# Kernel tuning notes

Hardware: AMD Instinct MI355X
Metric: run time of the kernel (lower is better)

## Reference

```python
import jax, jax.numpy as jnp
import numpy as np

B, L, DIM, K, V = 512, 200, 256, 2048, 100000


def setup_inputs() -> dict:
    key = jax.random.key(0)
    k1, k2, k3, k4, k5 = jax.random.split(key, 5)
    return {
        "history_item_ids": jax.random.randint(k1, (B, L), 0, V, dtype=jnp.int32),
        "history_item_masks": jax.random.randint(k2, (B, L), 0, 3, dtype=jnp.int32),
        "embedding_table": jax.random.normal(k3, (V, DIM), dtype=jnp.float32) * 0.1,
        "code_book": jax.random.normal(k4, (K, DIM), dtype=jnp.float32) * 0.1,
        "W_enc": jax.random.normal(k5, (2 * DIM, DIM), dtype=jnp.float32) * 0.05,
        "b_enc": jnp.zeros((DIM,), dtype=jnp.float32),
    }


def reference(history_item_ids, history_item_masks, embedding_table, code_book, W_enc, b_enc):
    # mask: valid history positions (>= 1)
    mask = (history_item_masks >= 1).astype(jnp.float32)            # [B, L]
    emb = embedding_table[history_item_ids] * mask[:, :, None]      # [B, L, D]
    # masked mean over history (eps matches the tf 1e-9)
    hist_mean = emb.sum(axis=1) / (mask.sum(axis=1, keepdims=True) + 1e-9)  # [B, D]
    # VQ quantization: pairwise squared distances, argmin, codebook gather
    flat = emb.reshape(-1, emb.shape[-1])                           # [B*L, D]
    distances = (
        jnp.sum(flat * flat, axis=1, keepdims=True)
        + jnp.sum(code_book * code_book, axis=1)
        - 2.0 * flat @ code_book.T
    )                                                               # [B*L, K]
    idx = jnp.argmin(distances, axis=1)                             # [B*L]
    vq = code_book[idx].reshape(emb.shape)                          # [B, L, D] (== one_hot @ code_book)
    vq_mean = vq.sum(axis=1) / mask.sum(axis=-1)[:, None]           # [B, D] (no eps in tf vqvae)
    x = jnp.concatenate([vq_mean, hist_mean], axis=-1)              # [B, 2D]
    return x @ W_enc + b_enc                                        # encoder dense -> [B, D]
```

## Files before the change

kernel.cpp:

```cpp
#include <hip/hip_runtime.h>
#include <hip/hip_bf16.h>
#include <cstddef>
#include <cstdint>

#define B_  512
#define L_  200
#define D_  256
#define K_  2048
#define BL_ (B_ * L_)

typedef __bf16 bf16x8 __attribute__((ext_vector_type(8)));
typedef float  f32x16 __attribute__((ext_vector_type(16)));

#define GL_LDS(g, l) __builtin_amdgcn_global_load_lds(                          \
    (const __attribute__((address_space(1))) void*)(g),                         \
    (__attribute__((address_space(3))) void*)(l), 16, 0, 0)

__device__ inline ushort f2bf(float f) {
    union { float f; uint u; } a; a.f = f;
    uint r = a.u + 0x7FFFu + ((a.u >> 16) & 1u);
    return (ushort)(r >> 16);
}

__global__ __launch_bounds__(256) void prep_kernel(const float* __restrict__ cb,
                                                   float* __restrict__ cnorm,
                                                   float* __restrict__ cnormR,
                                                   ushort* __restrict__ cbbf) {
    int code = (blockIdx.x * 256 + threadIdx.x) >> 6;
    int lane = threadIdx.x & 63;
    float4 v = ((const float4*)(cb + (size_t)code * D_))[lane];
    float s = v.x * v.x + v.y * v.y + v.z * v.z + v.w * v.w;
    #pragma unroll
    for (int off = 32; off; off >>= 1) s += __shfl_down(s, off);
    union { ushort us[4]; uint2 u2; } pk;
    pk.us[0] = f2bf(v.x); pk.us[1] = f2bf(v.y); pk.us[2] = f2bf(v.z); pk.us[3] = f2bf(v.w);
    ((uint2*)(cbbf + (size_t)code * D_))[lane] = pk.u2;
    if (lane == 0) {
        cnorm[code] = s;
        int r = code & 31;
        int h = (r >> 2) & 1;
        int j = (r & 3) | ((r >> 3) << 2);
        cnormR[(code & ~31) | (h << 4) | j] = s + 16.0f;
    }
}

__global__ __launch_bounds__(256) void kstar_kernel(const float* __restrict__ cnorm,
                                                    int* __restrict__ kstar) {
    __shared__ unsigned long long red[4];
    const int t = threadIdx.x;
    unsigned long long best = ~0ull;
    #pragma unroll
    for (int i = 0; i < K_ / 256; ++i) {
        int k = i * 256 + t;
        unsigned long long key = (((unsigned long long)__float_as_uint(cnorm[k])) << 11) | (unsigned)k;
        best = best < key ? best : key;
    }
    #pragma unroll
    for (int off = 32; off; off >>= 1) {
        unsigned long long o = __shfl_down(best, off);
        best = best < o ? best : o;
    }
    if ((t & 63) == 0) red[t >> 6] = best;
    __syncthreads();
    if (t == 0) {
        unsigned long long b = red[0];
        for (int i = 1; i < 4; ++i) b = b < red[i] ? b : red[i];
        kstar[0] = (int)(b & 0x7FFull);
    }
}

struct CN4 { float4 a, b, c, d; };

__device__ inline CN4 ldcn(const float* p) {
    CN4 r;
    r.a = ((const float4*)p)[0];
    r.b = ((const float4*)p)[1];
    r.c = ((const float4*)p)[2];
    r.d = ((const float4*)p)[3];
    return r;
}

#define STAGE(CIDX, BASE) {                                                     \
    int wub = __builtin_amdgcn_readfirstlane((t >> 6) * 256);                   \
    _Pragma("unroll")                                                           \
    for (int i_ = 0; i_ < 4; ++i_) {                                            \
      int slot = wub + i_ * 64 + (t & 63);                                      \
      int n_ = slot >> 5, up_ = slot & 31;                                      \
      int u_ = up_ ^ (n_ & 7);                                                  \
      GL_LDS(cbbf + (((size_t)(((CIDX) << 5) + n_)) << 8) + (u_ << 3),          \
             (char*)(BASE) + (size_t)(wub + i_ * 64) * 16);                     \
    } }

#define STAGE2(DI, BASE) {                                                      \
    STAGE(2 * (DI),     (char*)(BASE));                                         \
    STAGE(2 * (DI) + 1, (char*)(BASE) + 16384); }

#define ACCINIT(CN, A) {                                                        \
    A[0]=(CN).a.x; A[1]=(CN).a.y; A[2]=(CN).a.z; A[3]=(CN).a.w;                 \
    A[4]=(CN).b.x; A[5]=(CN).b.y; A[6]=(CN).b.z; A[7]=(CN).b.w;                 \
    A[8]=(CN).c.x; A[9]=(CN).c.y; A[10]=(CN).c.z; A[11]=(CN).c.w;               \
    A[12]=(CN).d.x; A[13]=(CN).d.y; A[14]=(CN).d.z; A[15]=(CN).d.w; }

#define SELR(NC, A0, A1) {                                                      \
    uint sb_ = (uint)((NC) << 5);                                               \
    _Pragma("unroll")                                                           \
    for (int jp_ = 0; jp_ < 8; ++jp_) {                                         \
      int j0_ = 2 * jp_, j1_ = 2 * jp_ + 1;                                     \
      uint c0_ = sb_ + (uint)((j0_ & 3) + 8 * (j0_ >> 2));                      \
      uint c1_ = sb_ + (uint)((j1_ & 3) + 8 * (j1_ >> 2));                      \
      {                                                                         \
        uint ka = (__float_as_uint(A0[j0_]) & 0xFFFFF800u) | (c0_ + h4);        \
        uint kb = (__float_as_uint(A0[j1_]) & 0xFFFFF800u) | (c1_ + h4);        \
        uint lo = min(ka, kb), hi = max(ka, kb);                                \
        uint tt = max(b1a, lo);                                                 \
        b1a = min(b1a, lo);                                                     \
        b2a = min(min(b2a, tt), hi);                                            \
      }                                                                         \
      {                                                                         \
        uint ka = (__float_as_uint(A1[j0_]) & 0xFFFFF800u) | (c0_ + h4);        \
        uint kb = (__float_as_uint(A1[j1_]) & 0xFFFFF800u) | (c1_ + h4);        \
        uint lo = min(ka, kb), hi = max(ka, kb);                                \
        uint tt = max(b1b, lo);                                                 \
        b1b = min(b1b, lo);                                                     \
        b2b = min(min(b2b, tt), hi);                                            \
      }                                                                         \
    } }

#define PROCSEL2(BASE, NC) {                                                    \
    CN4 cnX = ldcn(cnormR + ((NC) << 5) + h * 16);                              \
    CN4 cnY = ldcn(cnormR + (((NC) + 1) << 5) + h * 16);                        \
    f32x16 A0, A1, C0, C1;                                                      \
    ACCINIT(cnX, A0); A1 = A0;                                                  \
    ACCINIT(cnY, C0); C1 = C0;                                                  \
    _Pragma("unroll")                                                           \
    for (int s_ = 0; s_ < 16; ++s_) {                                           \
      int off_ = ((l31 << 5) + ((2 * s_ + h) ^ swz)) << 4;                      \
      bf16x8 aF = *(const bf16x8*)((const char*)(BASE) + off_);                 \
      bf16x8 aG = *(const bf16x8*)((const char*)(BASE) + 16384 + off_);         \
      A0 = __builtin_amdgcn_mfma_f32_32x32x16_bf16(aF, bfrag[0][s_], A0, 0,0,0);\
      A1 = __builtin_amdgcn_mfma_f32_32x32x16_bf16(aF, bfrag[1][s_], A1, 0,0,0);\
      C0 = __builtin_amdgcn_mfma_f32_32x32x16_bf16(aG, bfrag[0][s_], C0, 0,0,0);\
      C1 = __builtin_amdgcn_mfma_f32_32x32x16_bf16(aG, bfrag[1][s_], C1, 0,0,0);\
    }                                                                           \
    SELR((NC), A0, A1);                                                         \
    SELR((NC) + 1, C0, C1); }

__global__ __launch_bounds__(256, 2) void gemm_top2_kernel(
    const int* __restrict__ ids, const int* __restrict__ masks,
    const float* __restrict__ table, const ushort* __restrict__ cbbf,
    const float* __restrict__ cnormR, uint2* __restrict__ cand) {

  __shared__ ushort cbuf0[2 * 32 * 256];
  __shared__ ushort cbuf1[2 * 32 * 256];

  const int t    = threadIdx.x;
  const int lane = t & 63;
  const int l31  = lane & 31;
  const int h    = lane >> 5;
  const int w    = t >> 6;
  const int ptile = blockIdx.x;
  const int swz  = l31 & 7;
  const uint h4  = (uint)(h << 2);

  STAGE2(0, cbuf0);

  bf16x8 bfrag[2][16];
  #pragma unroll
  for (int pt = 0; pt < 2; ++pt) {
    int pos = ptile * 256 + w * 64 + pt * 32 + l31;
    int id  = ids[pos];
    float m = (masks[pos] >= 1) ? -2.0f : 0.0f;
    const float* er = table + (size_t)id * D_ + 8 * h;
    #pragma unroll
    for (int s = 0; s < 16; ++s) {
      float4 x = *(const float4*)(er + 16 * s);
      float4 y = *(const float4*)(er + 16 * s + 4);
      bf16x8 b;
      b[0] = (__bf16)(x.x * m); b[1] = (__bf16)(x.y * m);
      b[2] = (__bf16)(x.z * m); b[3] = (__bf16)(x.w * m);
      b[4] = (__bf16)(y.x * m); b[5] = (__bf16)(y.y * m);
      b[6] = (__bf16)(y.z * m); b[7] = (__bf16)(y.w * m);
      bfrag[pt][s] = b;
    }
  }

  uint b1a = 0xFFFFFFFFu, b2a = 0xFFFFFFFFu;
  uint b1b = 0xFFFFFFFFu, b2b = 0xFFFFFFFFu;

  __syncthreads();

  #pragma unroll 1
  for (int dt = 0; dt < 32; dt += 2) {
    STAGE2(dt + 1, cbuf1);
    PROCSEL2(cbuf0, dt * 2);
    __syncthreads();
    if (dt + 2 < 32) STAGE2(dt + 2, cbuf0);
    PROCSEL2(cbuf1, dt * 2 + 2);
    __syncthreads();
  }

  {
    uint ob1 = __shfl_xor(b1a, 32), ob2 = __shfl_xor(b2a, 32);
    uint m1 = min(b1a, ob1);
    uint m2 = min(min(max(b1a, ob1), b2a), ob2);
    if (h == 0) cand[(size_t)(ptile * 256 + w * 64 + 0 * 32 + l31)] = make_uint2(m1, m2);
  }
  {
    uint ob1 = __shfl_xor(b1b, 32), ob2 = __shfl_xor(b2b, 32);
    uint m1 = min(b1b, ob1);
    uint m2 = min(min(max(b1b, ob1), b2b), ob2);
    if (h == 0) cand[(size_t)(ptile * 256 + w * 64 + 1 * 32 + l31)] = make_uint2(m1, m2);
  }
}

#define GRP 5

__global__ __launch_bounds__(256, 1) void tail_kernel(
    const int* __restrict__ ids, const int* __restrict__ masks,
    const float* __restrict__ table, const float* __restrict__ cb,
    const float* __restrict__ cnorm, const uint2* __restrict__ cand2,
    const int* __restrict__ kstar,
    float* __restrict__ gacc, int* __restrict__ gcnt) {

    __shared__ float red_vq[4][D_];
    __shared__ float red_e[4][D_];
    __shared__ int   redc[4];

    const int b    = blockIdx.x >> 1;
    const int half = blockIdx.x & 1;
    const int t = threadIdx.x;
    const int wv = t >> 6, lane = t & 63;

    const int ks = kstar[0];
    float4 ckstar = ((const float4*)(cb + (size_t)ks * D_))[lane];

    float4 vqa = make_float4(0.f, 0.f, 0.f, 0.f);
    float4 ea  = make_float4(0.f, 0.f, 0.f, 0.f);
    int cnta = 0, mcnt = 0;

    #pragma unroll 1
    for (int g = 0; g < 25 / GRP; ++g) {
        const int l0 = half * 100 + wv * 25 + g * GRP;

        uint2 kk[GRP];
        int   id[GRP];
        int   mk[GRP];
        #pragma unroll
        for (int j = 0; j < GRP; ++j) {
            int u = b * L_ + l0 + j;
            kk[j] = cand2[u];
            id[j] = ids[u];
            mk[j] = masks[u];
        }

        int k1[GRP], k2[GRP];
        bool valid[GRP], needy[GRP];
        #pragma unroll
        for (int j = 0; j < GRP; ++j) {
            uint g1 = kk[j].x;
            uint g2 = kk[j].y;
            k1[j] = (int)(g1 & 0x7FFu);
            k2[j] = (int)(g2 & 0x7FFu);
            valid[j] = (mk[j] >= 1);
            needy[j] = valid[j] && (((g2 & 0xFFFFF800u) - (g1 & 0xFFFFF800u)) < (3u << 11));
        }

        float4 e[GRP], c1[GRP], c2[GRP];
        #pragma unroll
        for (int j = 0; j < GRP; ++j)
            if (valid[j]) e[j] = ((const float4*)(table + (size_t)id[j] * D_))[lane];
        #pragma unroll
        for (int j = 0; j < GRP; ++j)
            if (valid[j]) c1[j] = ((const float4*)(cb + (size_t)k1[j] * D_))[lane];
        #pragma unroll
        for (int j = 0; j < GRP; ++j)
            if (needy[j]) c2[j] = ((const float4*)(cb + (size_t)k2[j] * D_))[lane];

        #pragma unroll
        for (int j = 0; j < GRP; ++j) {
            if (!valid[j]) { mcnt++; continue; }
            float4 ch = c1[j];
            if (needy[j]) {
                float d1 = fmaf(e[j].x, c1[j].x, fmaf(e[j].y, c1[j].y,
                            fmaf(e[j].z, c1[j].z, e[j].w * c1[j].w)));
                float d2 = fmaf(e[j].x, c2[j].x, fmaf(e[j].y, c2[j].y,
                            fmaf(e[j].z, c2[j].z, e[j].w * c2[j].w)));
                #pragma unroll
                for (int off = 32; off; off >>= 1) {
                    d1 += __shfl_xor(d1, off);
                    d2 += __shfl_xor(d2, off);
                }
                float s1 = cnorm[k1[j]] - 2.0f * d1;
                float s2 = cnorm[k2[j]] - 2.0f * d2;
                bool sel = (s2 < s1) || (s2 == s1 && k2[j] < k1[j]);
                ch = sel ? c2[j] : c1[j];
            }
            vqa.x += ch.x; vqa.y += ch.y; vqa.z += ch.z; vqa.w += ch.w;
            ea.x += e[j].x; ea.y += e[j].y; ea.z += e[j].z; ea.w += e[j].w;
            cnta++;
        }
    }

    float fm = (float)mcnt;
    vqa.x = fmaf(fm, ckstar.x, vqa.x);
    vqa.y = fmaf(fm, ckstar.y, vqa.y);
    vqa.z = fmaf(fm, ckstar.z, vqa.z);
    vqa.w = fmaf(fm, ckstar.w, vqa.w);

    *(float4*)&red_vq[wv][lane * 4] = vqa;
    *(float4*)&red_e[wv][lane * 4]  = ea;
    if (lane == 0) redc[wv] = cnta;
    __syncthreads();

    float vs = red_vq[0][t] + red_vq[1][t] + red_vq[2][t] + red_vq[3][t];
    float es = red_e[0][t] + red_e[1][t] + red_e[2][t] + red_e[3][t];
    atomicAdd(&gacc[(size_t)b * (2 * D_) + t], vs);
    atomicAdd(&gacc[(size_t)b * (2 * D_) + D_ + t], es);
    if (t == 0) atomicAdd(&gcnt[b], redc[0] + redc[1] + redc[2] + redc[3]);
}

__global__ __launch_bounds__(256) void dense_kernel(
    const float* __restrict__ gacc, const int* __restrict__ gcnt,
    const float* __restrict__ W, const float* __restrict__ bvec,
    float* __restrict__ out) {

    __shared__ float x[2 * D_];
    const int b = blockIdx.x;
    const int t = threadIdx.x;

    float fc = (float)gcnt[b];
    x[t]      = gacc[(size_t)b * (2 * D_) + t] / fc;
    x[D_ + t] = gacc[(size_t)b * (2 * D_) + D_ + t] / (fc + 1e-9f);
    __syncthreads();

    float acc = bvec[t];
    #pragma unroll 8
    for (int i = 0; i < 2 * D_; ++i)
        acc = fmaf(x[i], W[i * D_ + t], acc);
    out[(size_t)b * D_ + t] = acc;
}

extern "C" void kernel_launch(void* const* d_in, const int* in_sizes, int n_in,
                              void* d_out, int out_size, void* d_ws, size_t ws_size,
                              hipStream_t stream) {
    const int*   ids   = (const int*)  d_in[0];
    const int*   masks = (const int*)  d_in[1];
    const float* table = (const float*)d_in[2];
    const float* cb    = (const float*)d_in[3];
    const float* W     = (const float*)d_in[4];
    const float* bvec  = (const float*)d_in[5];
    float* out = (float*)d_out;

    char* p = (char*)d_ws;
    float*  cnorm  = (float*)p;             p += 8192;
    float*  cnormR = (float*)p;             p += 8192;
    ushort* cbbf   = (ushort*)p;            p += 1048576;
    uint2*  cand   = (uint2*)p;             p += (size_t)BL_ * 16;
    float*  gacc   = (float*)p;             p += (size_t)B_ * 2 * D_ * 4;
    int*    gcnt   = (int*)p;               p += B_ * 4;
    int*    kstar  = (int*)p;               p += 64;

    hipMemsetAsync(gacc, 0, (size_t)B_ * 2 * D_ * 4 + B_ * 4, stream);

    prep_kernel<<<K_ * 64 / 256, 256, 0, stream>>>(cb, cnorm, cnormR, cbbf);
    kstar_kernel<<<1, 256, 0, stream>>>(cnorm, kstar);
    gemm_top2_kernel<<<BL_ / 256, 256, 0, stream>>>(ids, masks, table, cbbf, cnormR, cand);
    tail_kernel<<<B_ * 2, 256, 0, stream>>>(ids, masks, table, cb, cnorm,
                                            cand, kstar, gacc, gcnt);
    dense_kernel<<<B_, 256, 0, stream>>>(gacc, gcnt, W, bvec, out);
}
```

Before: 358.2 us.

## Split GEMM-top2 work across 8 waves and stage codebook norms in LDS

Each block of the codebook-distance GEMM now runs 512 threads (8 waves) instead of 256. Each wave handles 32 positions instead of 64, which halves the per-wave B fragments and accumulators and so cuts register pressure enough to raise occupancy. The codebook staging work is split across the extra waves, and the codebook norms are loaded once into LDS rather than read from global memory on every tile. The cost is that each codebook tile loaded into LDS feeds fewer MFMAs per wave, so LDS read traffic per FLOP goes up.

```diff
diff --git a/kernel.cpp b/kernel.cpp
--- a/kernel.cpp
+++ b/kernel.cpp
@@ -71,19 +71,10 @@
 
 struct CN4 { float4 a, b, c, d; };
 
-__device__ inline CN4 ldcn(const float* p) {
-    CN4 r;
-    r.a = ((const float4*)p)[0];
-    r.b = ((const float4*)p)[1];
-    r.c = ((const float4*)p)[2];
-    r.d = ((const float4*)p)[3];
-    return r;
-}
-
 #define STAGE(CIDX, BASE) {                                                     \
-    int wub = __builtin_amdgcn_readfirstlane((t >> 6) * 256);                   \
+    int wub = __builtin_amdgcn_readfirstlane((t >> 6) * 128);                   \
     _Pragma("unroll")                                                           \
-    for (int i_ = 0; i_ < 4; ++i_) {                                            \
+    for (int i_ = 0; i_ < 2; ++i_) {                                            \
       int slot = wub + i_ * 64 + (t & 63);                                      \
       int n_ = slot >> 5, up_ = slot & 31;                                      \
       int u_ = up_ ^ (n_ & 7);                                                  \
@@ -95,63 +86,56 @@
     STAGE(2 * (DI),     (char*)(BASE));                                         \
     STAGE(2 * (DI) + 1, (char*)(BASE) + 16384); }
 
+#define LDCN_LDS(NC, CN) {                                                      \
+    const float4* cp_ = (const float4*)(cnlds + ((NC) << 5) + (h << 4));        \
+    (CN).a = cp_[0]; (CN).b = cp_[1]; (CN).c = cp_[2]; (CN).d = cp_[3]; }
+
 #define ACCINIT(CN, A) {                                                        \
     A[0]=(CN).a.x; A[1]=(CN).a.y; A[2]=(CN).a.z; A[3]=(CN).a.w;                 \
     A[4]=(CN).b.x; A[5]=(CN).b.y; A[6]=(CN).b.z; A[7]=(CN).b.w;                 \
     A[8]=(CN).c.x; A[9]=(CN).c.y; A[10]=(CN).c.z; A[11]=(CN).c.w;               \
     A[12]=(CN).d.x; A[13]=(CN).d.y; A[14]=(CN).d.z; A[15]=(CN).d.w; }
 
-#define SELR(NC, A0, A1) {                                                      \
+#define SELR(NC, A) {                                                           \
     uint sb_ = (uint)((NC) << 5);                                               \
     _Pragma("unroll")                                                           \
     for (int jp_ = 0; jp_ < 8; ++jp_) {                                         \
       int j0_ = 2 * jp_, j1_ = 2 * jp_ + 1;                                     \
       uint c0_ = sb_ + (uint)((j0_ & 3) + 8 * (j0_ >> 2));                      \
       uint c1_ = sb_ + (uint)((j1_ & 3) + 8 * (j1_ >> 2));                      \
-      {                                                                         \
-        uint ka = (__float_as_uint(A0[j0_]) & 0xFFFFF800u) | (c0_ + h4);        \
-        uint kb = (__float_as_uint(A0[j1_]) & 0xFFFFF800u) | (c1_ + h4);        \
-        uint lo = min(ka, kb), hi = max(ka, kb);                                \
-        uint tt = max(b1a, lo);                                                 \
-        b1a = min(b1a, lo);                                                     \
-        b2a = min(min(b2a, tt), hi);                                            \
-      }                                                                         \
-      {                                                                         \
-        uint ka = (__float_as_uint(A1[j0_]) & 0xFFFFF800u) | (c0_ + h4);        \
-        uint kb = (__float_as_uint(A1[j1_]) & 0xFFFFF800u) | (c1_ + h4);        \
-        uint lo = min(ka, kb), hi = max(ka, kb);                                \
-        uint tt = max(b1b, lo);                                                 \
-        b1b = min(b1b, lo);                                                     \
-        b2b = min(min(b2b, tt), hi);                                            \
-      }                                                                         \
+      uint ka = (__float_as_uint(A[j0_]) & 0xFFFFF800u) | (c0_ + h4);           \
+      uint kb = (__float_as_uint(A[j1_]) & 0xFFFFF800u) | (c1_ + h4);           \
+      uint lo = min(ka, kb), hi = max(ka, kb);                                  \
+      uint tt = max(b1a, lo);                                                   \
+      b1a = min(b1a, lo);                                                       \
+      b2a = min(min(b2a, tt), hi);                                              \
     } }
 
-#define PROCSEL2(BASE, NC) {                                                    \
-    CN4 cnX = ldcn(cnormR + ((NC) << 5) + h * 16);                              \
-    CN4 cnY = ldcn(cnormR + (((NC) + 1) << 5) + h * 16);                        \
-    f32x16 A0, A1, C0, C1;                                                      \
-    ACCINIT(cnX, A0); A1 = A0;                                                  \
-    ACCINIT(cnY, C0); C1 = C0;                                                  \
+#define PROC2(BASE, NC) {                                                       \
+    CN4 cnX; LDCN_LDS((NC), cnX);                                               \
+    CN4 cnY; LDCN_LDS((NC) + 1, cnY);                                           \
+    f32x16 A0, C0;                                                              \
+    ACCINIT(cnX, A0);                                                           \
+    ACCINIT(cnY, C0);                                                           \
     _Pragma("unroll")                                                           \
     for (int s_ = 0; s_ < 16; ++s_) {                                           \
       int off_ = ((l31 << 5) + ((2 * s_ + h) ^ swz)) << 4;                      \
       bf16x8 aF = *(const bf16x8*)((const char*)(BASE) + off_);                 \
       bf16x8 aG = *(const bf16x8*)((const char*)(BASE) + 16384 + off_);         \
-      A0 = __builtin_amdgcn_mfma_f32_32x32x16_bf16(aF, bfrag[0][s_], A0, 0,0,0);\
-      A1 = __builtin_amdgcn_mfma_f32_32x32x16_bf16(aF, bfrag[1][s_], A1, 0,0,0);\
-      C0 = __builtin_amdgcn_mfma_f32_32x32x16_bf16(aG, bfrag[0][s_], C0, 0,0,0);\
-      C1 = __builtin_amdgcn_mfma_f32_32x32x16_bf16(aG, bfrag[1][s_], C1, 0,0,0);\
+      A0 = __builtin_amdgcn_mfma_f32_32x32x16_bf16(aF, bfrag[s_], A0, 0,0,0);   \
+      C0 = __builtin_amdgcn_mfma_f32_32x32x16_bf16(aG, bfrag[s_], C0, 0,0,0);   \
     }                                                                           \
-    SELR((NC), A0, A1);                                                         \
-    SELR((NC) + 1, C0, C1); }
-
-__global__ __launch_bounds__(256, 2) void gemm_top2_kernel(
+    SELR((NC), A0);                                                             \
+    SELR((NC) + 1, C0); }
+
+__global__ __launch_bounds__(512, 4) void gemm_top2_kernel(
     const int* __restrict__ ids, const int* __restrict__ masks,
     const float* __restrict__ table, const ushort* __restrict__ cbbf,
     const float* __restrict__ cnormR, uint2* __restrict__ cand) {
 
   __shared__ ushort cbuf0[2 * 32 * 256];
   __shared__ ushort cbuf1[2 * 32 * 256];
+  __shared__ float  cnlds[2048];
 
   const int t    = threadIdx.x;
   const int lane = t & 63;
@@ -163,11 +147,14 @@
   const uint h4  = (uint)(h << 2);
 
   STAGE2(0, cbuf0);
-
-  bf16x8 bfrag[2][16];
-  #pragma unroll
-  for (int pt = 0; pt < 2; ++pt) {
-    int pos = ptile * 256 + w * 64 + pt * 32 + l31;
+  {
+    int wub2 = __builtin_amdgcn_readfirstlane(w * 64);
+    GL_LDS(cnormR + (size_t)(wub2 + lane) * 4, (char*)cnlds + (size_t)wub2 * 16);
+  }
+
+  bf16x8 bfrag[16];
+  {
+    int pos = ptile * 256 + w * 32 + l31;
     int id  = ids[pos];
     float m = (masks[pos] >= 1) ? -2.0f : 0.0f;
     const float* er = table + (size_t)id * D_ + 8 * h;
@@ -180,22 +167,21 @@
       b[2] = (__bf16)(x.z * m); b[3] = (__bf16)(x.w * m);
       b[4] = (__bf16)(y.x * m); b[5] = (__bf16)(y.y * m);
       b[6] = (__bf16)(y.z * m); b[7] = (__bf16)(y.w * m);
-      bfrag[pt][s] = b;
+      bfrag[s] = b;
     }
   }
 
   uint b1a = 0xFFFFFFFFu, b2a = 0xFFFFFFFFu;
-  uint b1b = 0xFFFFFFFFu, b2b = 0xFFFFFFFFu;
 
   __syncthreads();
 
   #pragma unroll 1
-  for (int dt = 0; dt < 32; dt += 2) {
-    STAGE2(dt + 1, cbuf1);
-    PROCSEL2(cbuf0, dt * 2);
-    __syncthreads();
-    if (dt + 2 < 32) STAGE2(dt + 2, cbuf0);
-    PROCSEL2(cbuf1, dt * 2 + 2);
+  for (int p = 0; p < 32; p += 2) {
+    STAGE2(p + 1, cbuf1);
+    PROC2(cbuf0, p * 2);
+    __syncthreads();
+    if (p + 2 < 32) STAGE2(p + 2, cbuf0);
+    PROC2(cbuf1, p * 2 + 2);
     __syncthreads();
   }
 
@@ -203,13 +189,7 @@
     uint ob1 = __shfl_xor(b1a, 32), ob2 = __shfl_xor(b2a, 32);
     uint m1 = min(b1a, ob1);
     uint m2 = min(min(max(b1a, ob1), b2a), ob2);
-    if (h == 0) cand[(size_t)(ptile * 256 + w * 64 + 0 * 32 + l31)] = make_uint2(m1, m2);
-  }
-  {
-    uint ob1 = __shfl_xor(b1b, 32), ob2 = __shfl_xor(b2b, 32);
-    uint m1 = min(b1b, ob1);
-    uint m2 = min(min(max(b1b, ob1), b2b), ob2);
-    if (h == 0) cand[(size_t)(ptile * 256 + w * 64 + 1 * 32 + l31)] = make_uint2(m1, m2);
+    if (h == 0) cand[(size_t)(ptile * 256 + w * 32 + l31)] = make_uint2(m1, m2);
   }
 }
 
@@ -364,7 +344,7 @@
 
     prep_kernel<<<K_ * 64 / 256, 256, 0, stream>>>(cb, cnorm, cnormR, cbbf);
     kstar_kernel<<<1, 256, 0, stream>>>(cnorm, kstar);
-    gemm_top2_kernel<<<BL_ / 256, 256, 0, stream>>>(ids, masks, table, cbbf, cnormR, cand);
+    gemm_top2_kernel<<<BL_ / 256, 512, 0, stream>>>(ids, masks, table, cbbf, cnormR, cand);
     tail_kernel<<<B_ * 2, 256, 0, stream>>>(ids, masks, table, cb, cnorm,
                                             cand, kstar, gacc, gcnt);
     dense_kernel<<<B_, 256, 0, stream>>>(gacc, gcnt, W, bvec, out);
```

After: 323.7 us. -9.6%, faster.
